# Performance work log

Hardware: AMD Instinct MI355X
Metric: run time of the kernel (lower is better)

The kernel has to match this reference:

```python
import jax, jax.numpy as jnp
import numpy as np

V, E, L = 32000, 512, 2  # vocab_size, n_embd (== hidden), n_layer
B, T = 8, 1024


def setup_inputs() -> dict:
    key = jax.random.key(0)
    ks = jax.random.split(key, 6)
    inp = jax.random.randint(ks[0], (B, T), 0, V)
    wte = jax.random.normal(ks[1], (V, E), dtype=jnp.float32) * 0.02
    # PyTorch LSTM params per layer: weight_ih [4H, in], weight_hh [4H, H], b_ih [4H], b_hh [4H]
    W_ih = jax.random.normal(ks[2], (L, 4 * E, E), dtype=jnp.float32) * 0.04
    W_hh = jax.random.normal(ks[3], (L, 4 * E, E), dtype=jnp.float32) * 0.04
    b_ih = jnp.zeros((L, 4 * E), dtype=jnp.float32)
    b_hh = jnp.zeros((L, 4 * E), dtype=jnp.float32)
    fc_w = jax.random.normal(ks[4], (V, E), dtype=jnp.float32) * 0.02
    fc_b = jnp.zeros((V,), dtype=jnp.float32)
    return {"inp": inp, "wte": wte, "W_ih": W_ih, "W_hh": W_hh,
            "b_ih": b_ih, "b_hh": b_hh, "fc_w": fc_w, "fc_b": fc_b}


def _lstm_stack(x, W_ih, W_hh, b_ih, b_hh):
    # x: [B, T, E]; multi-layer LSTM, zero initial (h, c), PyTorch gate order i,f,g,o
    H = W_hh.shape[-1]
    n_layers = W_ih.shape[0]
    for l in range(n_layers):
        # input-to-hidden part is time-parallel: precompute once per layer
        xg = jnp.einsum('bte,ge->btg', x, W_ih[l]) + b_ih[l] + b_hh[l]  # [B,T,4H]
        Whh = W_hh[l]
        h0 = jnp.zeros((x.shape[0], H), x.dtype)
        c0 = jnp.zeros((x.shape[0], H), x.dtype)

        def step(carry, xg_t, Whh=Whh):
            h, c = carry
            g = xg_t + h @ Whh.T  # [B,4H]
            i, f, gg, o = jnp.split(g, 4, axis=-1)
            c = jax.nn.sigmoid(f) * c + jax.nn.sigmoid(i) * jnp.tanh(gg)
            h = jax.nn.sigmoid(o) * jnp.tanh(c)
            return (h, c), h

        (_, _), hs = jax.lax.scan(step, (h0, c0), jnp.swapaxes(xg, 0, 1))  # hs: [T,B,H]
        x = jnp.swapaxes(hs, 0, 1)  # [B,T,H] feeds next layer
    return x


def reference(inp, wte, W_ih, W_hh, b_ih, b_hh, fc_w, fc_b):
    x = wte[inp]  # [B,T,E] embedding lookup
    h = _lstm_stack(x, W_ih, W_hh, b_ih, b_hh)  # [B,T,H]
    logits = jnp.einsum('bth,vh->btv', h, fc_w) + fc_b  # [B,T,V]
    return logits
```

## Files before the change

kernel.cpp:

```cpp
#include <hip/hip_runtime.h>
#include <stdint.h>

typedef __attribute__((ext_vector_type(4))) float f32x4;
typedef __attribute__((ext_vector_type(8))) short s16x8;
typedef __attribute__((ext_vector_type(4))) unsigned short u16x4;

#define T_SEQ 1024
#define HID 512
#define SU 516

__device__ __forceinline__ unsigned short f2bf(float f) {
  uint32_t u = __float_as_uint(f);
  u += 0x7fffu + ((u >> 16) & 1u);
  return (unsigned short)(u >> 16);
}
__device__ __forceinline__ float sigf(float x) { return 1.f / (1.f + __expf(-x)); }
__device__ __forceinline__ float tanhfast(float x) {
  float e = __expf(2.f * x);
  return (e - 1.f) / (e + 1.f);
}

#define ALOAD(p) __hip_atomic_load((p), __ATOMIC_RELAXED, __HIP_MEMORY_SCOPE_AGENT)
#define ASTORE(p, v) __hip_atomic_store((p), (v), __ATOMIC_RELAXED, __HIP_MEMORY_SCOPE_AGENT)

#define GLL(gp, lp)                                                      \
  __builtin_amdgcn_global_load_lds(                                     \
      (const __attribute__((address_space(1))) void*)(gp),              \
      (__attribute__((address_space(3))) void*)(lp), 16, 0, 0)

__global__ __launch_bounds__(256) void embed_kernel(const int* __restrict__ inp,
                                                    const float* __restrict__ wte,
                                                    unsigned short* __restrict__ xbf) {
  const int m = blockIdx.x;
  const int idx = inp[m];
  const float* src = wte + (size_t)idx * HID;
  unsigned short* dst = xbf + (size_t)m * HID;
  const int e = threadIdx.x;
  dst[e] = f2bf(src[e]);
  dst[e + 256] = f2bf(src[e + 256]);
}

__global__ __launch_bounds__(256) void cvt_bf16_kernel(const float* __restrict__ src,
                                                       unsigned short* __restrict__ dst,
                                                       int n4) {
  const int i = blockIdx.x * 256 + threadIdx.x;
  if (i >= n4) return;
  f32x4 v = ((const f32x4*)src)[i];
  u16x4 o;
  o.x = f2bf(v.x); o.y = f2bf(v.y); o.z = f2bf(v.z); o.w = f2bf(v.w);
  ((u16x4*)dst)[i] = o;
}

__global__ __launch_bounds__(256) void bias_sum_kernel(const float* __restrict__ a,
                                                       const float* __restrict__ b,
                                                       float* __restrict__ o, int n) {
  const int i = blockIdx.x * 256 + threadIdx.x;
  if (i < n) o[i] = a[i] + b[i];
}

template <int MODE>
__global__ __launch_bounds__(256) void gemm_bt(const unsigned short* __restrict__ A,
                                               const unsigned short* __restrict__ B,
                                               float* __restrict__ C,
                                               const float* __restrict__ bias,
                                               int M, int N, int K) {
  __shared__ unsigned short As[128 * 32];
  __shared__ unsigned short Bs[128 * 32];
  const int nTiles = N >> 7;
  const int mt = blockIdx.x / nTiles;
  const int nt = blockIdx.x - mt * nTiles;
  const int m0 = mt << 7, n0 = nt << 7;
  const int tid = threadIdx.x;
  const int wave = tid >> 6, lane = tid & 63;
  const int wm = wave >> 1, wn = wave & 1;

  const int c1 = wave * 64 + lane;
  const int c2 = 256 + c1;
  const unsigned short* gA1 = A + (size_t)(m0 + (c1 >> 2)) * K + (c1 & 3) * 8;
  const unsigned short* gA2 = A + (size_t)(m0 + (c2 >> 2)) * K + (c2 & 3) * 8;
  const unsigned short* gB1 = B + (size_t)(n0 + (c1 >> 2)) * K + (c1 & 3) * 8;
  const unsigned short* gB2 = B + (size_t)(n0 + (c2 >> 2)) * K + (c2 & 3) * 8;
  unsigned short* lA1 = As + wave * 512;
  unsigned short* lA2 = As + 2048 + wave * 512;
  unsigned short* lB1 = Bs + wave * 512;
  unsigned short* lB2 = Bs + 2048 + wave * 512;

  f32x4 acc[4][4] = {};
  const int row_lo = lane & 15;
  const int kq = (lane >> 4) * 8;

  for (int k0 = 0; k0 < K; k0 += 32) {
    GLL(gA1 + k0, lA1);
    GLL(gA2 + k0, lA2);
    GLL(gB1 + k0, lB1);
    GLL(gB2 + k0, lB2);
    __syncthreads();
    s16x8 af[4], bfr[4];
#pragma unroll
    for (int f = 0; f < 4; ++f) {
      af[f] = *(const s16x8*)(As + (wm * 64 + f * 16 + row_lo) * 32 + kq);
      bfr[f] = *(const s16x8*)(Bs + (wn * 64 + f * 16 + row_lo) * 32 + kq);
    }
#pragma unroll
    for (int i = 0; i < 4; ++i)
#pragma unroll
      for (int j = 0; j < 4; ++j)
        acc[i][j] = __builtin_amdgcn_mfma_f32_16x16x32_bf16(af[i], bfr[j], acc[i][j], 0, 0, 0);
    __syncthreads();
  }

  float bv[4];
#pragma unroll
  for (int j = 0; j < 4; ++j) bv[j] = bias[n0 + wn * 64 + j * 16 + row_lo];
  const int rbase = (lane >> 4) * 4;
#pragma unroll
  for (int i = 0; i < 4; ++i) {
#pragma unroll
    for (int r = 0; r < 4; ++r) {
      const int m = m0 + wm * 64 + i * 16 + rbase + r;
      const size_t row = MODE == 1 ? ((size_t)(m & 7) * T_SEQ + (m >> 3))
                       : MODE == 2 ? ((size_t)(m & (T_SEQ - 1)) * 8 + (m >> 10))
                                   : (size_t)m;
      float* cp = C + row * (size_t)N;
#pragma unroll
      for (int j = 0; j < 4; ++j) cp[n0 + wn * 64 + j * 16 + row_lo] = acc[i][j][r] + bv[j];
    }
  }
}

template <bool IS_L1, int KTW>
__device__ __forceinline__ void lstm_body(
    int u0, int tid,
    const float* __restrict__ xg1t,
    const unsigned short* __restrict__ Wa,
    const unsigned short* __restrict__ Wb,
    const float* __restrict__ b_ih, const float* __restrict__ b_hh,
    unsigned int* __restrict__ h1bf, unsigned int* __restrict__ h2bf,
    int* cnt1, int* cnt2,
    unsigned int* HBLu, f32x4* CLred, float* CP, float* XG) {
  const int wave = tid >> 6, lane = tid & 63;
  const int nt = wave & 1, kh = wave >> 1;
  const int col = lane & 15, grp = lane >> 4;

  const int wrow = nt * 16 + col;
  const int grow = (wrow >> 3) * 512 + u0 + (wrow & 7);
  s16x8 bfrag[KTW];
#pragma unroll
  for (int f = 0; f < KTW; ++f) {
    const int kt = kh * KTW + f;
    const unsigned short* W = (IS_L1 || kt < 16) ? Wa : Wb;
    const int kk = (IS_L1 ? kt : (kt & 15)) * 32;
    bfrag[f] = *(const s16x8*)(W + (size_t)grow * 512 + kk + grp * 8);
  }

  const int pb = lane >> 3, puu = lane & 7;
  float cst = 0.f;
  float bias_g[4] = {0.f, 0.f, 0.f, 0.f};
  if (!IS_L1 && wave == 0) {
#pragma unroll
    for (int g = 0; g < 4; ++g) {
      const int gr = 2048 + g * 512 + u0 + puu;
      bias_g[g] = b_ih[gr] + b_hh[gr];
    }
  }

  const unsigned short* hb = (const unsigned short*)HBLu;
  const int arow = lane & 7;

  for (int t = 0; t < T_SEQ; ++t) {
    if (tid == 0) {
      if (IS_L1) {
        if (t > 0)
          while (ALOAD(cnt1) < 64 * t) __builtin_amdgcn_s_sleep(1);
      } else {
        while (ALOAD(cnt1) < 64 * (t + 1)) __builtin_amdgcn_s_sleep(1);
        if (t > 0)
          while (ALOAD(cnt2) < 64 * t) __builtin_amdgcn_s_sleep(1);
      }
    }
    __syncthreads();

#pragma unroll
    for (int i = 0; i < 8; ++i) {
      const int d = tid + 256 * i;
      const int row = d >> 8, c8 = d & 255;
      if (IS_L1) {
        unsigned int v = 0;
        if (t > 0) v = ALOAD(h1bf + (size_t)(t - 1) * 2048 + row * 256 + c8);
        HBLu[row * SU + c8] = v;
      } else {
        HBLu[row * SU + c8] = ALOAD(h1bf + (size_t)t * 2048 + row * 256 + c8);
        unsigned int v2 = 0;
        if (t > 0) v2 = ALOAD(h2bf + (size_t)(t - 1) * 2048 + row * 256 + c8);
        HBLu[row * SU + 256 + c8] = v2;
      }
    }
    if (IS_L1)
      XG[tid] = xg1t[(size_t)(t * 8 + (tid >> 5)) * 2048 + ((tid >> 3) & 3) * 512 + u0 + (tid & 7)];
    __syncthreads();

    f32x4 aA = {}, aB = {};
#pragma unroll
    for (int f = 0; f < KTW; f += 2) {
      const int kt0 = kh * KTW + f;
      s16x8 a0 = *(const s16x8*)(hb + arow * (SU * 2) + kt0 * 32 + grp * 8);
      s16x8 a1 = *(const s16x8*)(hb + arow * (SU * 2) + (kt0 + 1) * 32 + grp * 8);
      aA = __builtin_amdgcn_mfma_f32_16x16x32_bf16(a0, bfrag[f], aA, 0, 0, 0);
      aB = __builtin_amdgcn_mfma_f32_16x16x32_bf16(a1, bfrag[f + 1], aB, 0, 0, 0);
    }
    f32x4 acc = aA + aB;

    if (kh == 1) CLred[nt * 64 + lane] = acc;
    __syncthreads();
    if (kh == 0) {
      acc += CLred[nt * 64 + lane];
      if (grp < 2) {
#pragma unroll
        for (int q = 0; q < 4; ++q) CP[nt * 128 + col * 8 + (grp * 4 + q)] = acc[q];
      }
    }
    __syncthreads();

    if (wave == 0) {
      float gi = CP[puu * 8 + pb];
      float gf = CP[(8 + puu) * 8 + pb];
      float gg = CP[128 + puu * 8 + pb];
      float go = CP[128 + (8 + puu) * 8 + pb];
      if (IS_L1) {
        gi += XG[pb * 32 + puu];       gf += XG[pb * 32 + 8 + puu];
        gg += XG[pb * 32 + 16 + puu];  go += XG[pb * 32 + 24 + puu];
      } else {
        gi += bias_g[0]; gf += bias_g[1]; gg += bias_g[2]; go += bias_g[3];
      }
      cst = sigf(gf) * cst + sigf(gi) * tanhfast(gg);
      const float hv = sigf(go) * tanhfast(cst);
      const unsigned int hb16 = f2bf(hv);
      const unsigned int partner = (unsigned int)__shfl_xor((int)hb16, 1);
      if ((puu & 1) == 0) {
        unsigned int pack = (hb16 & 0xffffu) | (partner << 16);
        unsigned int* dst = (IS_L1 ? h1bf : h2bf) + (size_t)(t * 8 + pb) * 256 + ((u0 + puu) >> 1);
        ASTORE(dst, pack);
      }
      asm volatile("s_waitcnt vmcnt(0)" ::: "memory");
      if (lane == 0)
        __hip_atomic_fetch_add(IS_L1 ? cnt1 : cnt2, 1, __ATOMIC_RELAXED, __HIP_MEMORY_SCOPE_AGENT);
    }
  }
}

__global__ __launch_bounds__(256) void lstm_kernel(
    const float* __restrict__ xg1t,
    const unsigned short* __restrict__ wihbf,
    const unsigned short* __restrict__ whhbf,
    const float* __restrict__ b_ih, const float* __restrict__ b_hh,
    unsigned int* __restrict__ h1bf, unsigned int* __restrict__ h2bf,
    int* __restrict__ cnt) {
  __shared__ unsigned int HBLu[8 * SU];
  __shared__ f32x4 CLred[128];
  __shared__ float CP[256];
  __shared__ float XG[256];
  const int wg = blockIdx.x, tid = threadIdx.x;
  if (wg < 64)
    lstm_body<true, 8>(wg * 8, tid, xg1t, whhbf, nullptr, b_ih, b_hh,
                       h1bf, h2bf, cnt, cnt + 64, HBLu, CLred, CP, XG);
  else
    lstm_body<false, 16>((wg - 64) * 8, tid, xg1t,
                         wihbf + (size_t)2048 * 512, whhbf + (size_t)2048 * 512,
                         b_ih, b_hh, h1bf, h2bf, cnt, cnt + 64, HBLu, CLred, CP, XG);
}

extern "C" void kernel_launch(void* const* d_in, const int* in_sizes, int n_in,
                              void* d_out, int out_size, void* d_ws, size_t ws_size,
                              hipStream_t stream) {
  (void)in_sizes; (void)n_in; (void)out_size; (void)ws_size;
  const int* inp = (const int*)d_in[0];
  const float* wte = (const float*)d_in[1];
  const float* W_ih = (const float*)d_in[2];
  const float* W_hh = (const float*)d_in[3];
  const float* b_ih = (const float*)d_in[4];
  const float* b_hh = (const float*)d_in[5];
  const float* fc_w = (const float*)d_in[6];
  const float* fc_b = (const float*)d_in[7];
  float* out = (float*)d_out;

  char* ob = (char*)d_out;
  float* xg1t = (float*)(ob);
  unsigned int* h1bf = (unsigned int*)(ob + (64u << 20));
  unsigned short* whh_bf = (unsigned short*)(ob + (72u << 20));
  unsigned short* wih_bf = (unsigned short*)(ob + (76u << 20));
  unsigned short* x_bf = (unsigned short*)(ob + (80u << 20));

  char* ws = (char*)d_ws;
  unsigned short* fcw_bf = (unsigned short*)(ws);
  float* bias12 = (float*)(ws + (32u << 20));
  int* cnt = (int*)(ws + (33u << 20));
  unsigned int* h2bf = (unsigned int*)(ws + (35u << 20));

  hipMemsetAsync(cnt, 0, 512, stream);
  embed_kernel<<<8192, 256, 0, stream>>>(inp, wte, x_bf);
  cvt_bf16_kernel<<<2048, 256, 0, stream>>>(W_ih, wih_bf, 2 * 2048 * 512 / 4);
  cvt_bf16_kernel<<<2048, 256, 0, stream>>>(W_hh, whh_bf, 2 * 2048 * 512 / 4);
  cvt_bf16_kernel<<<16000, 256, 0, stream>>>(fc_w, fcw_bf, 32000 * 512 / 4);
  bias_sum_kernel<<<8, 256, 0, stream>>>(b_ih, b_hh, bias12, 2048);
  gemm_bt<2><<<64 * 16, 256, 0, stream>>>(x_bf, wih_bf, xg1t, bias12, 8192, 2048, 512);
  lstm_kernel<<<128, 256, 0, stream>>>(xg1t, wih_bf, whh_bf, b_ih, b_hh, h1bf, h2bf, cnt);
  gemm_bt<1><<<64 * 250, 256, 0, stream>>>((const unsigned short*)h2bf, fcw_bf, out, fc_b,
                                           8192, 32000, 512);
}
```

Baseline: 5.763 ms.

## Restructure LSTM recurrence: per-block flags, direct register A-fragments, fewer workgroups

The persistent LSTM kernel drops from 128 to 64 workgroups, each now owning 16 hidden units with one wave per gate and the full K range kept in registers, so the cross-wave LDS reduction and one barrier per step go away. A-fragments of h are loaded straight from global memory into registers with atomic 64-bit loads instead of being staged through LDS. The single shared atomic counter is replaced by per-workgroup flags that a whole wave polls in parallel with a ballot, and the second layer reads a precomputed summed bias. The intent is to shorten the latency of each serial timestep; the cost is heavier register pressure and fewer CUs working on each step.

New measurement: 9.832 ms. +70.6%, slower.

```diff
diff --git a/kernel.cpp b/kernel.cpp
--- a/kernel.cpp
+++ b/kernel.cpp
@@ -4,10 +4,10 @@
 typedef __attribute__((ext_vector_type(4))) float f32x4;
 typedef __attribute__((ext_vector_type(8))) short s16x8;
 typedef __attribute__((ext_vector_type(4))) unsigned short u16x4;
+typedef unsigned long long u64c;
 
 #define T_SEQ 1024
 #define HID 512
-#define SU 516
 
 __device__ __forceinline__ unsigned short f2bf(float f) {
   uint32_t u = __float_as_uint(f);
@@ -22,6 +22,11 @@
 
 #define ALOAD(p) __hip_atomic_load((p), __ATOMIC_RELAXED, __HIP_MEMORY_SCOPE_AGENT)
 #define ASTORE(p, v) __hip_atomic_store((p), (v), __ATOMIC_RELAXED, __HIP_MEMORY_SCOPE_AGENT)
+
+union frag_u { u64c q[2]; s16x8 v; };
+__device__ __forceinline__ s16x8 zero_frag() {
+  frag_u f; f.q[0] = 0; f.q[1] = 0; return f.v;
+}
 
 #define GLL(gp, lp)                                                      \
   __builtin_amdgcn_global_load_lds(                                     \
@@ -128,145 +133,168 @@
   }
 }
 
-template <bool IS_L1, int KTW>
-__device__ __forceinline__ void lstm_body(
-    int u0, int tid,
+template <bool IS_L1>
+__device__ __forceinline__ void lstm_side(
+    int wg, int tid,
     const float* __restrict__ xg1t,
     const unsigned short* __restrict__ Wa,
     const unsigned short* __restrict__ Wb,
-    const float* __restrict__ b_ih, const float* __restrict__ b_hh,
+    const float* __restrict__ bias2,
     unsigned int* __restrict__ h1bf, unsigned int* __restrict__ h2bf,
-    int* cnt1, int* cnt2,
-    unsigned int* HBLu, f32x4* CLred, float* CP, float* XG) {
+    unsigned int* __restrict__ flags1, unsigned int* __restrict__ flags2,
+    float* GT) {
+  constexpr int NKT = IS_L1 ? 16 : 32;
   const int wave = tid >> 6, lane = tid & 63;
-  const int nt = wave & 1, kh = wave >> 1;
   const int col = lane & 15, grp = lane >> 4;
-
-  const int wrow = nt * 16 + col;
-  const int grow = (wrow >> 3) * 512 + u0 + (wrow & 7);
-  s16x8 bfrag[KTW];
-#pragma unroll
-  for (int f = 0; f < KTW; ++f) {
-    const int kt = kh * KTW + f;
-    const unsigned short* W = (IS_L1 || kt < 16) ? Wa : Wb;
-    const int kk = (IS_L1 ? kt : (kt & 15)) * 32;
-    bfrag[f] = *(const s16x8*)(W + (size_t)grow * 512 + kk + grp * 8);
-  }
-
-  const int pb = lane >> 3, puu = lane & 7;
-  float cst = 0.f;
-  float bias_g[4] = {0.f, 0.f, 0.f, 0.f};
-  if (!IS_L1 && wave == 0) {
-#pragma unroll
-    for (int g = 0; g < 4; ++g) {
-      const int gr = 2048 + g * 512 + u0 + puu;
-      bias_g[g] = b_ih[gr] + b_hh[gr];
-    }
-  }
-
-  const unsigned short* hb = (const unsigned short*)HBLu;
-  const int arow = lane & 7;
+  const int u0 = wg * 16;
+  const int koff = grp * 8;
+  const int ab = lane & 7;
+
+  s16x8 bfr[NKT];
+  {
+    const int grow = wave * 512 + u0 + col;
+#pragma unroll
+    for (int kt = 0; kt < NKT; ++kt) {
+      const unsigned short* W = (IS_L1 || kt < 16) ? Wa : Wb;
+      const int kk = (kt & 15) * 32 + koff;
+      bfr[kt] = *(const s16x8*)(W + (size_t)grow * 512 + kk);
+    }
+  }
+
+  const int pb = lane & 7, ps = lane >> 3;
+  float bias_g[2][4];
+  if constexpr (!IS_L1) {
+    if (wave == 0) {
+#pragma unroll
+      for (int r = 0; r < 2; ++r)
+#pragma unroll
+        for (int g = 0; g < 4; ++g)
+          bias_g[r][g] = bias2[g * 512 + u0 + r * 8 + ps];
+    }
+  }
+  float c0 = 0.f, c1 = 0.f;
+
+  unsigned int* myflag = (IS_L1 ? flags1 : flags2) + wg * 16;
+  const unsigned int* pollp =
+      IS_L1 ? (flags1 + (lane & 31) * 16)
+            : (lane < 32 ? flags1 + lane * 16 : flags2 + (lane - 32) * 16);
 
   for (int t = 0; t < T_SEQ; ++t) {
-    if (tid == 0) {
-      if (IS_L1) {
-        if (t > 0)
-          while (ALOAD(cnt1) < 64 * t) __builtin_amdgcn_s_sleep(1);
+    float xv[2][4];
+    if constexpr (IS_L1) {
+      if (wave == 0) {
+#pragma unroll
+        for (int r = 0; r < 2; ++r)
+#pragma unroll
+          for (int g = 0; g < 4; ++g)
+            xv[r][g] = xg1t[(size_t)(t * 8 + pb) * 2048 + g * 512 + u0 + r * 8 + ps];
+      }
+    }
+    if (!IS_L1 || t > 0) {
+      const unsigned int tgt =
+          IS_L1 ? (unsigned)t : (lane < 32 ? (unsigned)(t + 1) : (unsigned)t);
+      while (true) {
+        unsigned int v = ALOAD(pollp);
+        if (__ballot(v >= tgt) == ~0ULL) break;
+        __builtin_amdgcn_s_sleep(1);
+      }
+    }
+    s16x8 afr[NKT];
+    if constexpr (IS_L1) {
+      if (t > 0) {
+        const u64c* hp =
+            (const u64c*)((const unsigned short*)h1bf + ((size_t)(t - 1) * 8 + ab) * 512 + koff);
+#pragma unroll
+        for (int kt = 0; kt < 16; ++kt) {
+          frag_u f; f.q[0] = ALOAD(hp + kt * 8); f.q[1] = ALOAD(hp + kt * 8 + 1);
+          afr[kt] = f.v;
+        }
       } else {
-        while (ALOAD(cnt1) < 64 * (t + 1)) __builtin_amdgcn_s_sleep(1);
-        if (t > 0)
-          while (ALOAD(cnt2) < 64 * t) __builtin_amdgcn_s_sleep(1);
-      }
-    }
+#pragma unroll
+        for (int kt = 0; kt < 16; ++kt) afr[kt] = zero_frag();
+      }
+    } else {
+      const u64c* hp1 =
+          (const u64c*)((const unsigned short*)h1bf + ((size_t)t * 8 + ab) * 512 + koff);
+#pragma unroll
+      for (int kt = 0; kt < 16; ++kt) {
+        frag_u f; f.q[0] = ALOAD(hp1 + kt * 8); f.q[1] = ALOAD(hp1 + kt * 8 + 1);
+        afr[kt] = f.v;
+      }
+      if (t > 0) {
+        const u64c* hp2 =
+            (const u64c*)((const unsigned short*)h2bf + ((size_t)(t - 1) * 8 + ab) * 512 + koff);
+#pragma unroll
+        for (int kt = 0; kt < 16; ++kt) {
+          frag_u f; f.q[0] = ALOAD(hp2 + kt * 8); f.q[1] = ALOAD(hp2 + kt * 8 + 1);
+          afr[16 + kt] = f.v;
+        }
+      } else {
+#pragma unroll
+        for (int kt = 16; kt < 32; ++kt) afr[kt] = zero_frag();
+      }
+    }
+    f32x4 a0 = {}, a1 = {}, a2 = {}, a3 = {};
+#pragma unroll
+    for (int kt = 0; kt < NKT; kt += 4) {
+      a0 = __builtin_amdgcn_mfma_f32_16x16x32_bf16(afr[kt], bfr[kt], a0, 0, 0, 0);
+      a1 = __builtin_amdgcn_mfma_f32_16x16x32_bf16(afr[kt + 1], bfr[kt + 1], a1, 0, 0, 0);
+      a2 = __builtin_amdgcn_mfma_f32_16x16x32_bf16(afr[kt + 2], bfr[kt + 2], a2, 0, 0, 0);
+      a3 = __builtin_amdgcn_mfma_f32_16x16x32_bf16(afr[kt + 3], bfr[kt + 3], a3, 0, 0, 0);
+    }
+    f32x4 acc = (a0 + a1) + (a2 + a3);
+    if (grp < 2) *(f32x4*)(GT + wave * 128 + col * 8 + grp * 4) = acc;
     __syncthreads();
-
-#pragma unroll
-    for (int i = 0; i < 8; ++i) {
-      const int d = tid + 256 * i;
-      const int row = d >> 8, c8 = d & 255;
-      if (IS_L1) {
-        unsigned int v = 0;
-        if (t > 0) v = ALOAD(h1bf + (size_t)(t - 1) * 2048 + row * 256 + c8);
-        HBLu[row * SU + c8] = v;
-      } else {
-        HBLu[row * SU + c8] = ALOAD(h1bf + (size_t)t * 2048 + row * 256 + c8);
-        unsigned int v2 = 0;
-        if (t > 0) v2 = ALOAD(h2bf + (size_t)(t - 1) * 2048 + row * 256 + c8);
-        HBLu[row * SU + 256 + c8] = v2;
-      }
-    }
-    if (IS_L1)
-      XG[tid] = xg1t[(size_t)(t * 8 + (tid >> 5)) * 2048 + ((tid >> 3) & 3) * 512 + u0 + (tid & 7)];
-    __syncthreads();
-
-    f32x4 aA = {}, aB = {};
-#pragma unroll
-    for (int f = 0; f < KTW; f += 2) {
-      const int kt0 = kh * KTW + f;
-      s16x8 a0 = *(const s16x8*)(hb + arow * (SU * 2) + kt0 * 32 + grp * 8);
-      s16x8 a1 = *(const s16x8*)(hb + arow * (SU * 2) + (kt0 + 1) * 32 + grp * 8);
-      aA = __builtin_amdgcn_mfma_f32_16x16x32_bf16(a0, bfrag[f], aA, 0, 0, 0);
-      aB = __builtin_amdgcn_mfma_f32_16x16x32_bf16(a1, bfrag[f + 1], aB, 0, 0, 0);
-    }
-    f32x4 acc = aA + aB;
-
-    if (kh == 1) CLred[nt * 64 + lane] = acc;
-    __syncthreads();
-    if (kh == 0) {
-      acc += CLred[nt * 64 + lane];
-      if (grp < 2) {
-#pragma unroll
-        for (int q = 0; q < 4; ++q) CP[nt * 128 + col * 8 + (grp * 4 + q)] = acc[q];
-      }
-    }
-    __syncthreads();
-
     if (wave == 0) {
-      float gi = CP[puu * 8 + pb];
-      float gf = CP[(8 + puu) * 8 + pb];
-      float gg = CP[128 + puu * 8 + pb];
-      float go = CP[128 + (8 + puu) * 8 + pb];
-      if (IS_L1) {
-        gi += XG[pb * 32 + puu];       gf += XG[pb * 32 + 8 + puu];
-        gg += XG[pb * 32 + 16 + puu];  go += XG[pb * 32 + 24 + puu];
-      } else {
-        gi += bias_g[0]; gf += bias_g[1]; gg += bias_g[2]; go += bias_g[3];
-      }
-      cst = sigf(gf) * cst + sigf(gi) * tanhfast(gg);
-      const float hv = sigf(go) * tanhfast(cst);
-      const unsigned int hb16 = f2bf(hv);
-      const unsigned int partner = (unsigned int)__shfl_xor((int)hb16, 1);
-      if ((puu & 1) == 0) {
-        unsigned int pack = (hb16 & 0xffffu) | (partner << 16);
-        unsigned int* dst = (IS_L1 ? h1bf : h2bf) + (size_t)(t * 8 + pb) * 256 + ((u0 + puu) >> 1);
-        ASTORE(dst, pack);
+      float hv[2];
+#pragma unroll
+      for (int r = 0; r < 2; ++r) {
+        const int u = r * 8 + ps;
+        float gi = GT[0 * 128 + u * 8 + pb];
+        float gf = GT[1 * 128 + u * 8 + pb];
+        float gg = GT[2 * 128 + u * 8 + pb];
+        float go = GT[3 * 128 + u * 8 + pb];
+        if constexpr (IS_L1) {
+          gi += xv[r][0]; gf += xv[r][1]; gg += xv[r][2]; go += xv[r][3];
+        } else {
+          gi += bias_g[r][0]; gf += bias_g[r][1]; gg += bias_g[r][2]; go += bias_g[r][3];
+        }
+        float& cc = r ? c1 : c0;
+        cc = sigf(gf) * cc + sigf(gi) * tanhfast(gg);
+        hv[r] = sigf(go) * tanhfast(cc);
+      }
+      unsigned int* hout = IS_L1 ? h1bf : h2bf;
+#pragma unroll
+      for (int r = 0; r < 2; ++r) {
+        unsigned int hb16 = f2bf(hv[r]);
+        unsigned int partner = (unsigned int)__shfl_xor((int)hb16, 8);
+        if ((ps & 1) == 0) {
+          unsigned int pack = (hb16 & 0xffffu) | (partner << 16);
+          ASTORE(hout + (size_t)(t * 8 + pb) * 256 + wg * 8 + r * 4 + (ps >> 1), pack);
+        }
       }
       asm volatile("s_waitcnt vmcnt(0)" ::: "memory");
-      if (lane == 0)
-        __hip_atomic_fetch_add(IS_L1 ? cnt1 : cnt2, 1, __ATOMIC_RELAXED, __HIP_MEMORY_SCOPE_AGENT);
-    }
-  }
-}
-
-__global__ __launch_bounds__(256) void lstm_kernel(
+      if (lane == 0) ASTORE(myflag, (unsigned int)(t + 1));
+    }
+  }
+}
+
+__global__ __launch_bounds__(256, 1) void lstm_kernel(
     const float* __restrict__ xg1t,
-    const unsigned short* __restrict__ wihbf,
-    const unsigned short* __restrict__ whhbf,
-    const float* __restrict__ b_ih, const float* __restrict__ b_hh,
+    const unsigned short* __restrict__ whh1,
+    const unsigned short* __restrict__ wih2,
+    const unsigned short* __restrict__ whh2,
+    const float* __restrict__ bias2,
     unsigned int* __restrict__ h1bf, unsigned int* __restrict__ h2bf,
-    int* __restrict__ cnt) {
-  __shared__ unsigned int HBLu[8 * SU];
-  __shared__ f32x4 CLred[128];
-  __shared__ float CP[256];
-  __shared__ float XG[256];
+    unsigned int* __restrict__ flags) {
+  __shared__ float GT[512];
   const int wg = blockIdx.x, tid = threadIdx.x;
-  if (wg < 64)
-    lstm_body<true, 8>(wg * 8, tid, xg1t, whhbf, nullptr, b_ih, b_hh,
-                       h1bf, h2bf, cnt, cnt + 64, HBLu, CLred, CP, XG);
+  if (wg < 32)
+    lstm_side<true>(wg, tid, xg1t, whh1, nullptr, nullptr,
+                    h1bf, h2bf, flags, flags + 512, GT);
   else
-    lstm_body<false, 16>((wg - 64) * 8, tid, xg1t,
-                         wihbf + (size_t)2048 * 512, whhbf + (size_t)2048 * 512,
-                         b_ih, b_hh, h1bf, h2bf, cnt, cnt + 64, HBLu, CLred, CP, XG);
+    lstm_side<false>(wg - 32, tid, xg1t, wih2, whh2, bias2,
+                     h1bf, h2bf, flags, flags + 512, GT);
 }
 
 extern "C" void kernel_launch(void* const* d_in, const int* in_sizes, int n_in,
@@ -293,17 +321,19 @@
   char* ws = (char*)d_ws;
   unsigned short* fcw_bf = (unsigned short*)(ws);
   float* bias12 = (float*)(ws + (32u << 20));
-  int* cnt = (int*)(ws + (33u << 20));
+  unsigned int* flags = (unsigned int*)(ws + (33u << 20));
   unsigned int* h2bf = (unsigned int*)(ws + (35u << 20));
 
-  hipMemsetAsync(cnt, 0, 512, stream);
+  hipMemsetAsync(flags, 0, 4096, stream);
   embed_kernel<<<8192, 256, 0, stream>>>(inp, wte, x_bf);
   cvt_bf16_kernel<<<2048, 256, 0, stream>>>(W_ih, wih_bf, 2 * 2048 * 512 / 4);
   cvt_bf16_kernel<<<2048, 256, 0, stream>>>(W_hh, whh_bf, 2 * 2048 * 512 / 4);
   cvt_bf16_kernel<<<16000, 256, 0, stream>>>(fc_w, fcw_bf, 32000 * 512 / 4);
-  bias_sum_kernel<<<8, 256, 0, stream>>>(b_ih, b_hh, bias12, 2048);
+  bias_sum_kernel<<<16, 256, 0, stream>>>(b_ih, b_hh, bias12, 4096);
   gemm_bt<2><<<64 * 16, 256, 0, stream>>>(x_bf, wih_bf, xg1t, bias12, 8192, 2048, 512);
-  lstm_kernel<<<128, 256, 0, stream>>>(xg1t, wih_bf, whh_bf, b_ih, b_hh, h1bf, h2bf, cnt);
+  lstm_kernel<<<64, 256, 0, stream>>>(xg1t, whh_bf, wih_bf + (size_t)2048 * 512,
+                                      whh_bf + (size_t)2048 * 512, bias12 + 2048,
+                                      h1bf, h2bf, flags);
   gemm_bt<1><<<64 * 250, 256, 0, stream>>>((const unsigned short*)h2bf, fcw_bf, out, fc_b,
                                            8192, 32000, 512);
 }
```
